# Kernel tuning notes

Measured on AMD Instinct MI355X. Metric: run time of the kernel, lower is better.

## Reference

```python
import jax, jax.numpy as jnp
import numpy as np

# config matching init_kwargs
B, LQ, LKV = 2, 1024, 1024
H, DQK, DV = 8, 64, 64
DQ = DK = DVIN = DOUT = 512
SPAN, STRIDE = 128, 1


def setup_inputs() -> dict:
    key = jax.random.key(0)
    ks = jax.random.split(key, 7)
    q = jax.random.normal(ks[0], (B, LQ, DQ), jnp.float32)
    k = jax.random.normal(ks[1], (B, LKV, DK), jnp.float32)
    v = jax.random.normal(ks[2], (B, LKV, DVIN), jnp.float32)
    # nn.Linear(bias=False) weights, stored as [in, out] for x @ W
    Wq = jax.random.normal(ks[3], (DQ, H * DQK), jnp.float32) / np.sqrt(DQ).astype(np.float32)
    Wk = jax.random.normal(ks[4], (DK, H * DQK), jnp.float32) / np.sqrt(DK).astype(np.float32)
    Wv = jax.random.normal(ks[5], (DVIN, H * DV), jnp.float32) / np.sqrt(DVIN).astype(np.float32)
    Wo = jax.random.normal(ks[6], (H * DV, DOUT), jnp.float32) / np.sqrt(H * DV).astype(np.float32)
    return dict(q=q, k=k, v=v, Wq=Wq, Wk=Wk, Wv=Wv, Wo=Wo)


def reference(q, k, v, Wq, Wk, Wv, Wo):
    b = q.shape[0]
    Q = (q @ Wq).reshape(b, LQ, H, DQK).transpose(0, 2, 1, 3)    # [b,H,LQ,DQK]
    K = (k @ Wk).reshape(b, LKV, H, DQK).transpose(0, 2, 1, 3)   # [b,H,LKV,DQK]
    V = (v @ Wv).reshape(b, LKV, H, DV).transpose(0, 2, 1, 3)    # [b,H,LKV,DV]

    # banded window indices: kvi[i, j] = i - (span-1) + stride*j
    row = jnp.arange(SPAN)[:, None]
    col = jnp.arange(LQ)[None, :]
    kvi = row - (SPAN - 1) + STRIDE * col                         # [SPAN, LQ]
    valid = (kvi >= 0) & (kvi < LKV)
    kvi_c = jnp.clip(kvi, 0, LKV - 1)

    Kw = K[:, :, kvi_c, :]                                        # [b,H,SPAN,LQ,DQK]
    scores = jnp.einsum('bhjd,bhsjd->bhsj', Q, Kw) / np.float32(np.sqrt(DQK))
    scores = jnp.where(valid[None, None], scores, -jnp.inf)
    w = jax.nn.softmax(scores, axis=2)                            # softmax over span (dim=2)

    Vw = V[:, :, kvi_c, :]                                        # [b,H,SPAN,LQ,DV]
    out_h = jnp.einsum('bhsj,bhsjd->bhjd', w, Vw)                 # [b,H,LQ,DV]
    out = out_h.transpose(0, 2, 1, 3).reshape(b, LQ, H * DV)
    return out @ Wo
```

## Files before the change

kernel.cpp:

```cpp
#include <hip/hip_runtime.h>
#include <hip/hip_bf16.h>

#define LQ 1024
#define NH 8
#define DHEAD 64
#define DMODEL 512
#define SPAN 128
#define MROWS 2048

typedef __attribute__((ext_vector_type(8))) short   bf16x8;
typedef __attribute__((ext_vector_type(4))) float   f32x4;
typedef __attribute__((ext_vector_type(8))) unsigned short us8;

static __device__ __forceinline__ unsigned short f2bf(float f) {
    union { __hip_bfloat16 h; unsigned short u; } cv;
    cv.h = __float2bfloat16(f);
    return cv.u;
}

static __device__ __forceinline__ void gload_lds16(const void* g, void* l) {
    __builtin_amdgcn_global_load_lds((const __attribute__((address_space(1))) void*)g,
                                     (__attribute__((address_space(3))) void*)l, 16, 0, 0);
}

__global__ __launch_bounds__(256) void transposeW(
    const float* __restrict__ W0, const float* __restrict__ W1,
    const float* __restrict__ W2, const float* __restrict__ W3,
    unsigned short* __restrict__ T0, unsigned short* __restrict__ T1,
    unsigned short* __restrict__ T2, unsigned short* __restrict__ T3)
{
    const float* W = blockIdx.z == 0 ? W0 : blockIdx.z == 1 ? W1 : blockIdx.z == 2 ? W2 : W3;
    unsigned short* T = blockIdx.z == 0 ? T0 : blockIdx.z == 1 ? T1 : blockIdx.z == 2 ? T2 : T3;
    __shared__ unsigned short sT[64][72];
    int c = threadIdx.x & 63;
    int r0 = (threadIdx.x >> 6) * 16;
    int n0 = blockIdx.x * 64, k0 = blockIdx.y * 64;
    #pragma unroll
    for (int i = 0; i < 16; ++i) {
        int r = r0 + i;
        sT[c][r] = f2bf(W[(size_t)(k0 + r) * DMODEL + n0 + c]);
    }
    __syncthreads();
    #pragma unroll
    for (int i = 0; i < 16; ++i) {
        int r = r0 + i;
        T[(size_t)(n0 + r) * DMODEL + k0 + c] = sT[r][c];
    }
}

__global__ __launch_bounds__(512, 4) void gemm_qkv(
    const float* __restrict__ q, const float* __restrict__ k, const float* __restrict__ v,
    const unsigned short* __restrict__ WtQ, const unsigned short* __restrict__ WtK,
    const unsigned short* __restrict__ WtV,
    unsigned short* __restrict__ Qp, unsigned short* __restrict__ Kp,
    unsigned short* __restrict__ Vt)
{
    __shared__ __align__(16) unsigned short As[2][2][4096];
    __shared__ __align__(16) unsigned short Bs[2][2][4096];

    const int z = blockIdx.z;
    const float* A = z == 0 ? q : (z == 1 ? k : v);
    const unsigned short* Bt = z == 0 ? WtQ : (z == 1 ? WtK : WtV);
    unsigned short* C = z == 0 ? Qp : (z == 1 ? Kp : Vt);
    const bool mode2 = (z == 2);

    const int tid = threadIdx.x;
    const int lane = tid & 63;
    const int w = tid >> 6;
    const int wg = w & 3;
    const int half = w >> 2;
    const int tidh = tid & 255;
    const int wm = wg >> 1, wn = wg & 1;
    const int m0 = blockIdx.y * 64;
    const int n0 = blockIdx.x * 64;

    const int srow = lane >> 3;
    const int sgrp = (lane & 7) ^ srow;

    f32x4 acc[2][2];
    #pragma unroll
    for (int i = 0; i < 2; ++i)
        #pragma unroll
        for (int j = 0; j < 2; ++j)
            acc[i][j] = f32x4{0.f, 0.f, 0.f, 0.f};

    auto stageB = [&](int buf, int ktg) {
        const int k0 = ktg * 64;
        #pragma unroll
        for (int cc = 0; cc < 2; ++cc) {
            int call = wg * 2 + cc;
            int row = call * 8 + srow;
            gload_lds16(Bt + (size_t)(n0 + row) * DMODEL + k0 + (sgrp << 3),
                        &Bs[half][buf][call * 512]);
        }
    };

    float4 areg[2][2];
    auto loadA = [&](int ktg) {
        const int k0 = ktg * 64;
        #pragma unroll
        for (int i = 0; i < 2; ++i) {
            int c = i * 256 + tidh;
            int row = c >> 3, g = c & 7;
            const float* p = A + (size_t)(m0 + row) * DMODEL + k0 + g * 8;
            areg[i][0] = *(const float4*)p;
            areg[i][1] = *(const float4*)(p + 4);
        }
    };
    auto writeA = [&](int buf) {
        #pragma unroll
        for (int i = 0; i < 2; ++i) {
            int c = i * 256 + tidh;
            int row = c >> 3, g = c & 7;
            us8 t;
            t[0] = f2bf(areg[i][0].x); t[1] = f2bf(areg[i][0].y);
            t[2] = f2bf(areg[i][0].z); t[3] = f2bf(areg[i][0].w);
            t[4] = f2bf(areg[i][1].x); t[5] = f2bf(areg[i][1].y);
            t[6] = f2bf(areg[i][1].z); t[7] = f2bf(areg[i][1].w);
            *(us8*)&As[half][buf][row * 64 + ((g ^ (row & 7)) << 3)] = t;
        }
    };

    const int frow = lane & 15;
    const int fkg  = lane >> 4;

    auto ldfrag = [&](const unsigned short* base, int rb, int ks) -> bf16x8 {
        int row = rb * 16 + frow;
        int kg = ks * 4 + fkg;
        int off = row * 64 + ((kg ^ (row & 7)) << 3);
        return *(const bf16x8*)&base[off];
    };

    const unsigned short* aB[2] = { mode2 ? Bs[half][0] : As[half][0],
                                    mode2 ? Bs[half][1] : As[half][1] };
    const unsigned short* bB[2] = { mode2 ? As[half][0] : Bs[half][0],
                                    mode2 ? As[half][1] : Bs[half][1] };
    const int ra = mode2 ? wn : wm;
    const int rb_ = mode2 ? wm : wn;

    const int ktbase = half * 4;
    loadA(ktbase);
    stageB(0, ktbase);
    writeA(0);
    __syncthreads();

    for (int t = 0; t < 4; ++t) {
        int buf = t & 1;
        if (t < 3) { loadA(ktbase + t + 1); stageB(buf ^ 1, ktbase + t + 1); }
        #pragma unroll
        for (int ks = 0; ks < 2; ++ks) {
            bf16x8 a0 = ldfrag(aB[buf], ra * 2 + 0, ks);
            bf16x8 a1 = ldfrag(aB[buf], ra * 2 + 1, ks);
            bf16x8 b0 = ldfrag(bB[buf], rb_ * 2 + 0, ks);
            bf16x8 b1 = ldfrag(bB[buf], rb_ * 2 + 1, ks);
            acc[0][0] = __builtin_amdgcn_mfma_f32_16x16x32_bf16(a0, b0, acc[0][0], 0, 0, 0);
            acc[0][1] = __builtin_amdgcn_mfma_f32_16x16x32_bf16(a0, b1, acc[0][1], 0, 0, 0);
            acc[1][0] = __builtin_amdgcn_mfma_f32_16x16x32_bf16(a1, b0, acc[1][0], 0, 0, 0);
            acc[1][1] = __builtin_amdgcn_mfma_f32_16x16x32_bf16(a1, b1, acc[1][1], 0, 0, 0);
        }
        if (t < 3) writeA(buf ^ 1);
        __syncthreads();
    }

    float* red = (float*)&As[0][0][0];
    if (half == 1) {
        int base = (wg * 64 + lane) * 17;
        #pragma unroll
        for (int i = 0; i < 2; ++i)
            #pragma unroll
            for (int j = 0; j < 2; ++j)
                #pragma unroll
                for (int r = 0; r < 4; ++r)
                    red[base + (i * 2 + j) * 4 + r] = acc[i][j][r];
    }
    __syncthreads();
    if (half == 0) {
        int base = (wg * 64 + lane) * 17;
        #pragma unroll
        for (int i = 0; i < 2; ++i)
            #pragma unroll
            for (int j = 0; j < 2; ++j)
                #pragma unroll
                for (int r = 0; r < 4; ++r)
                    acc[i][j][r] += red[base + (i * 2 + j) * 4 + r];

        #pragma unroll
        for (int i = 0; i < 2; ++i) {
            #pragma unroll
            for (int j = 0; j < 2; ++j) {
                #pragma unroll
                for (int r = 0; r < 4; ++r) {
                    if (mode2) {
                        int n = n0 + wn * 32 + i * 16 + (lane >> 4) * 4 + r;
                        int m = m0 + wm * 32 + j * 16 + (lane & 15);
                        int b = m >> 10, jq = m & 1023, h = n >> 6, d = n & 63;
                        C[(((size_t)(b * NH + h) * DHEAD) + d) * LQ + jq] = f2bf(acc[i][j][r]);
                    } else {
                        int m = m0 + wm * 32 + i * 16 + (lane >> 4) * 4 + r;
                        int n = n0 + wn * 32 + j * 16 + (lane & 15);
                        int b = m >> 10, jq = m & 1023, h = n >> 6, d = n & 63;
                        C[(((size_t)(b * NH + h) * LQ) + jq) * DHEAD + d] = f2bf(acc[i][j][r]);
                    }
                }
            }
        }
    }
}

__global__ __launch_bounds__(512, 4) void gemm_out(
    const unsigned short* __restrict__ A, const unsigned short* __restrict__ Bt,
    float* __restrict__ C)
{
    __shared__ __align__(16) unsigned short As[2][2][2048];
    __shared__ __align__(16) unsigned short Bs[2][2][4096];

    const int tid = threadIdx.x;
    const int lane = tid & 63;
    const int w = tid >> 6;
    const int wg = w & 3;
    const int half = w >> 2;
    const int m0 = blockIdx.y * 32;
    const int n0 = blockIdx.x * 64;

    const int srow = lane >> 3;
    const int sgrp = (lane & 7) ^ srow;

    f32x4 acc[2];
    acc[0] = f32x4{0.f, 0.f, 0.f, 0.f};
    acc[1] = f32x4{0.f, 0.f, 0.f, 0.f};

    auto stage = [&](int buf, int ktg) {
        const int k0 = ktg * 64;
        gload_lds16(A + (size_t)(m0 + wg * 8 + srow) * DMODEL + k0 + (sgrp << 3),
                    &As[half][buf][wg * 512]);
        #pragma unroll
        for (int cc = 0; cc < 2; ++cc) {
            int call = wg * 2 + cc;
            int row = call * 8 + srow;
            gload_lds16(Bt + (size_t)(n0 + row) * DMODEL + k0 + (sgrp << 3),
                        &Bs[half][buf][call * 512]);
        }
    };

    const int frow = lane & 15;
    const int fkg  = lane >> 4;

    auto ldfrag = [&](const unsigned short* base, int rb, int ks) -> bf16x8 {
        int row = rb * 16 + frow;
        int kg = ks * 4 + fkg;
        int off = row * 64 + ((kg ^ (row & 7)) << 3);
        return *(const bf16x8*)&base[off];
    };

    const int ktbase = half * 4;
    stage(0, ktbase);
    __syncthreads();

    for (int t = 0; t < 4; ++t) {
        int buf = t & 1;
        if (t < 3) stage(buf ^ 1, ktbase + t + 1);
        #pragma unroll
        for (int ks = 0; ks < 2; ++ks) {
            bf16x8 a0 = ldfrag(As[half][buf], 0, ks);
            bf16x8 a1 = ldfrag(As[half][buf], 1, ks);
            bf16x8 b0 = ldfrag(Bs[half][buf], wg, ks);
            acc[0] = __builtin_amdgcn_mfma_f32_16x16x32_bf16(a0, b0, acc[0], 0, 0, 0);
            acc[1] = __builtin_amdgcn_mfma_f32_16x16x32_bf16(a1, b0, acc[1], 0, 0, 0);
        }
        __syncthreads();
    }

    float* red = (float*)&As[0][0][0];
    if (half == 1) {
        int base = (wg * 64 + lane) * 9;
        #pragma unroll
        for (int i = 0; i < 2; ++i)
            #pragma unroll
            for (int r = 0; r < 4; ++r)
                red[base + i * 4 + r] = acc[i][r];
    }
    __syncthreads();
    if (half == 0) {
        int base = (wg * 64 + lane) * 9;
        #pragma unroll
        for (int i = 0; i < 2; ++i) {
            #pragma unroll
            for (int r = 0; r < 4; ++r) {
                float vsum = acc[i][r] + red[base + i * 4 + r];
                int m = m0 + i * 16 + (lane >> 4) * 4 + r;
                int n = n0 + wg * 16 + (lane & 15);
                C[(size_t)m * DMODEL + n] = vsum;
            }
        }
    }
}

__global__ __launch_bounds__(256) void attn_mfma(
    const unsigned short* __restrict__ Qp, const unsigned short* __restrict__ Kp,
    const unsigned short* __restrict__ Vt, unsigned short* __restrict__ O)
{
    __shared__ __align__(16) unsigned short Ks[192 * 64];
    __shared__ __align__(16) unsigned short Vs[64 * 192];
    __shared__ __align__(16) unsigned short Ps[64 * 200];

    const int tid = threadIdx.x;
    const int lane = tid & 63;
    const int w = tid >> 6;
    const int bh = blockIdx.y;
    const int j0 = blockIdx.x * 64;
    const int kv0 = j0 - 128;

    const unsigned short* Kg = Kp + (size_t)bh * LQ * DHEAD;
    const unsigned short* Vg = Vt + (size_t)bh * DHEAD * LQ;

    const us8 zz = {0, 0, 0, 0, 0, 0, 0, 0};

    us8 kreg[6];
    #pragma unroll
    for (int i = 0; i < 6; ++i) {
        int c = i * 256 + tid;
        int row = c >> 3, g = c & 7;
        int grow = kv0 + row;
        us8 t = zz;
        if (grow >= 0) t = *(const us8*)&Kg[(size_t)grow * DHEAD + g * 8];
        kreg[i] = t;
    }
    us8 vreg[6];
    #pragma unroll
    for (int i = 0; i < 6; ++i) {
        int c = i * 256 + tid;
        int d = c / 24, g = c - d * 24;
        int col = kv0 + g * 8;
        us8 t = zz;
        if (col >= 0) t = *(const us8*)&Vg[(size_t)d * LQ + col];
        vreg[i] = t;
    }
    #pragma unroll
    for (int i = 0; i < 6; ++i) {
        int c = i * 256 + tid;
        int row = c >> 3, g = c & 7;
        *(us8*)&Ks[row * 64 + ((g ^ (row & 7)) << 3)] = kreg[i];
    }
    #pragma unroll
    for (int i = 0; i < 6; ++i) {
        int c = i * 256 + tid;
        int d = c / 24, g = c - d * 24;
        int sg = (g & ~7) | ((g & 7) ^ (d & 7));
        *(us8*)&Vs[d * 192 + sg * 8] = vreg[i];
    }

    const int frow = lane & 15, fkg = lane >> 4;

    bf16x8 qa[2];
    {
        const unsigned short* Qrow = Qp + ((size_t)bh * LQ + j0 + w * 16 + frow) * DHEAD;
        qa[0] = *(const bf16x8*)&Qrow[fkg * 8];
        qa[1] = *(const bf16x8*)&Qrow[32 + fkg * 8];
    }

    __syncthreads();

    f32x4 sacc[12];
    #pragma unroll
    for (int b = 0; b < 12; ++b) sacc[b] = f32x4{0.f, 0.f, 0.f, 0.f};
    #pragma unroll
    for (int b = 0; b < 12; ++b) {
        #pragma unroll
        for (int ks = 0; ks < 2; ++ks) {
            int row = b * 16 + frow;
            int kg = ks * 4 + fkg;
            bf16x8 kb = *(const bf16x8*)&Ks[row * 64 + ((kg ^ (row & 7)) << 3)];
            sacc[b] = __builtin_amdgcn_mfma_f32_16x16x32_bf16(qa[ks], kb, sacc[b], 0, 0, 0);
        }
    }

    #pragma unroll
    for (int r = 0; r < 4; ++r) {
        int q = w * 16 + fkg * 4 + r;
        float sv[12];
        float mx = -1e30f;
        #pragma unroll
        for (int b = 0; b < 12; ++b) {
            int rel = b * 16 + frow - 128 - q;
            int kvabs = kv0 + b * 16 + frow;
            bool valid = (rel <= 0) & (rel >= -(SPAN - 1)) & (kvabs >= 0);
            float s = valid ? sacc[b][r] * 0.125f : -1e30f;
            sv[b] = s;
            mx = fmaxf(mx, s);
        }
        #pragma unroll
        for (int off = 1; off < 16; off <<= 1) mx = fmaxf(mx, __shfl_xor(mx, off));
        float sum = 0.f;
        #pragma unroll
        for (int b = 0; b < 12; ++b) { float p = __expf(sv[b] - mx); sv[b] = p; sum += p; }
        #pragma unroll
        for (int off = 1; off < 16; off <<= 1) sum += __shfl_xor(sum, off);
        float inv = 1.0f / sum;
        #pragma unroll
        for (int b = 0; b < 12; ++b) sacc[b][r] = sv[b] * inv;
    }

    #pragma unroll
    for (int b = 0; b < 12; ++b) {
        #pragma unroll
        for (int r = 0; r < 4; ++r) {
            int q = w * 16 + fkg * 4 + r;
            Ps[q * 200 + b * 16 + frow] = f2bf(sacc[b][r]);
        }
    }

    f32x4 oacc[4];
    #pragma unroll
    for (int nb = 0; nb < 4; ++nb) oacc[nb] = f32x4{0.f, 0.f, 0.f, 0.f};
    #pragma unroll
    for (int kb = 0; kb < 6; ++kb) {
        int q = w * 16 + frow;
        bf16x8 pa = *(const bf16x8*)&Ps[q * 200 + (kb * 4 + fkg) * 8];
        #pragma unroll
        for (int nb = 0; nb < 4; ++nb) {
            int d = nb * 16 + frow;
            int g = kb * 4 + fkg;
            int sg = (g & ~7) | ((g & 7) ^ (d & 7));
            bf16x8 vb = *(const bf16x8*)&Vs[d * 192 + sg * 8];
            oacc[nb] = __builtin_amdgcn_mfma_f32_16x16x32_bf16(pa, vb, oacc[nb], 0, 0, 0);
        }
    }

    int b = bh >> 3, h = bh & 7;
    #pragma unroll
    for (int nb = 0; nb < 4; ++nb) {
        #pragma unroll
        for (int r = 0; r < 4; ++r) {
            int jq = j0 + w * 16 + fkg * 4 + r;
            int col = h * 64 + nb * 16 + frow;
            O[(size_t)(b * LQ + jq) * DMODEL + col] = f2bf(oacc[nb][r]);
        }
    }
}

extern "C" void kernel_launch(void* const* d_in, const int* in_sizes, int n_in,
                              void* d_out, int out_size, void* d_ws, size_t ws_size,
                              hipStream_t stream) {
    const float* q  = (const float*)d_in[0];
    const float* k  = (const float*)d_in[1];
    const float* v  = (const float*)d_in[2];
    const float* Wq = (const float*)d_in[3];
    const float* Wk = (const float*)d_in[4];
    const float* Wv = (const float*)d_in[5];
    const float* Wo = (const float*)d_in[6];

    const size_t MK = (size_t)MROWS * DMODEL;
    const size_t WK = (size_t)DMODEL * DMODEL;

    unsigned short* WtQ = (unsigned short*)d_ws;
    unsigned short* WtK = WtQ + WK;
    unsigned short* WtV = WtK + WK;
    unsigned short* WtO = WtV + WK;
    unsigned short* Qp  = WtO + WK;
    unsigned short* Kp  = Qp + MK;
    unsigned short* Vt  = Kp + MK;
    unsigned short* Ah  = Vt + MK;

    transposeW<<<dim3(8, 8, 4), 256, 0, stream>>>(Wq, Wk, Wv, Wo, WtQ, WtK, WtV, WtO);

    gemm_qkv<<<dim3(8, 32, 3), 512, 0, stream>>>(q, k, v, WtQ, WtK, WtV, Qp, Kp, Vt);

    attn_mfma<<<dim3(LQ / 64, 16), 256, 0, stream>>>(Qp, Kp, Vt, Ah);

    gemm_out<<<dim3(8, 64), 512, 0, stream>>>(Ah, WtO, (float*)d_out);
}
```

Baseline: 41.48 us.

## Fuse output projection into attention kernel via per-head atomic accumulation

Removes the separate output-projection GEMM. Each attention block now multiplies its per-head 64x64 output tile by the matching 64-row slice of Wo, reading the weights straight from global memory, and atomically adds the partial result into the fp32 output. The output buffer is zeroed with a memset beforehand. This drops one kernel launch and the bf16 round trip of the attention output. In exchange it adds 8-way atomic contention per output element, uncached global weight loads, a memset, and a large live accumulator array that raises register pressure.

New measurement: 71.82 us. 73.2% more time.

```diff
diff --git a/kernel.cpp b/kernel.cpp
--- a/kernel.cpp
+++ b/kernel.cpp
@@ -207,101 +207,15 @@
     }
 }
 
-__global__ __launch_bounds__(512, 4) void gemm_out(
-    const unsigned short* __restrict__ A, const unsigned short* __restrict__ Bt,
-    float* __restrict__ C)
-{
-    __shared__ __align__(16) unsigned short As[2][2][2048];
-    __shared__ __align__(16) unsigned short Bs[2][2][4096];
-
-    const int tid = threadIdx.x;
-    const int lane = tid & 63;
-    const int w = tid >> 6;
-    const int wg = w & 3;
-    const int half = w >> 2;
-    const int m0 = blockIdx.y * 32;
-    const int n0 = blockIdx.x * 64;
-
-    const int srow = lane >> 3;
-    const int sgrp = (lane & 7) ^ srow;
-
-    f32x4 acc[2];
-    acc[0] = f32x4{0.f, 0.f, 0.f, 0.f};
-    acc[1] = f32x4{0.f, 0.f, 0.f, 0.f};
-
-    auto stage = [&](int buf, int ktg) {
-        const int k0 = ktg * 64;
-        gload_lds16(A + (size_t)(m0 + wg * 8 + srow) * DMODEL + k0 + (sgrp << 3),
-                    &As[half][buf][wg * 512]);
-        #pragma unroll
-        for (int cc = 0; cc < 2; ++cc) {
-            int call = wg * 2 + cc;
-            int row = call * 8 + srow;
-            gload_lds16(Bt + (size_t)(n0 + row) * DMODEL + k0 + (sgrp << 3),
-                        &Bs[half][buf][call * 512]);
-        }
-    };
-
-    const int frow = lane & 15;
-    const int fkg  = lane >> 4;
-
-    auto ldfrag = [&](const unsigned short* base, int rb, int ks) -> bf16x8 {
-        int row = rb * 16 + frow;
-        int kg = ks * 4 + fkg;
-        int off = row * 64 + ((kg ^ (row & 7)) << 3);
-        return *(const bf16x8*)&base[off];
-    };
-
-    const int ktbase = half * 4;
-    stage(0, ktbase);
-    __syncthreads();
-
-    for (int t = 0; t < 4; ++t) {
-        int buf = t & 1;
-        if (t < 3) stage(buf ^ 1, ktbase + t + 1);
-        #pragma unroll
-        for (int ks = 0; ks < 2; ++ks) {
-            bf16x8 a0 = ldfrag(As[half][buf], 0, ks);
-            bf16x8 a1 = ldfrag(As[half][buf], 1, ks);
-            bf16x8 b0 = ldfrag(Bs[half][buf], wg, ks);
-            acc[0] = __builtin_amdgcn_mfma_f32_16x16x32_bf16(a0, b0, acc[0], 0, 0, 0);
-            acc[1] = __builtin_amdgcn_mfma_f32_16x16x32_bf16(a1, b0, acc[1], 0, 0, 0);
-        }
-        __syncthreads();
-    }
-
-    float* red = (float*)&As[0][0][0];
-    if (half == 1) {
-        int base = (wg * 64 + lane) * 9;
-        #pragma unroll
-        for (int i = 0; i < 2; ++i)
-            #pragma unroll
-            for (int r = 0; r < 4; ++r)
-                red[base + i * 4 + r] = acc[i][r];
-    }
-    __syncthreads();
-    if (half == 0) {
-        int base = (wg * 64 + lane) * 9;
-        #pragma unroll
-        for (int i = 0; i < 2; ++i) {
-            #pragma unroll
-            for (int r = 0; r < 4; ++r) {
-                float vsum = acc[i][r] + red[base + i * 4 + r];
-                int m = m0 + i * 16 + (lane >> 4) * 4 + r;
-                int n = n0 + wg * 16 + (lane & 15);
-                C[(size_t)m * DMODEL + n] = vsum;
-            }
-        }
-    }
-}
-
-__global__ __launch_bounds__(256) void attn_mfma(
+__global__ __launch_bounds__(256) void attn_out(
     const unsigned short* __restrict__ Qp, const unsigned short* __restrict__ Kp,
-    const unsigned short* __restrict__ Vt, unsigned short* __restrict__ O)
+    const unsigned short* __restrict__ Vt, const unsigned short* __restrict__ WtO,
+    float* __restrict__ out)
 {
     __shared__ __align__(16) unsigned short Ks[192 * 64];
     __shared__ __align__(16) unsigned short Vs[64 * 192];
     __shared__ __align__(16) unsigned short Ps[64 * 200];
+    __shared__ __align__(16) unsigned short Os[64][72];
 
     const int tid = threadIdx.x;
     const int lane = tid & 63;
@@ -426,14 +340,39 @@
         }
     }
 
-    int b = bh >> 3, h = bh & 7;
+    const int b = bh >> 3, h = bh & 7;
     #pragma unroll
     for (int nb = 0; nb < 4; ++nb) {
         #pragma unroll
         for (int r = 0; r < 4; ++r) {
-            int jq = j0 + w * 16 + fkg * 4 + r;
-            int col = h * 64 + nb * 16 + frow;
-            O[(size_t)(b * LQ + jq) * DMODEL + col] = f2bf(oacc[nb][r]);
+            int q = w * 16 + fkg * 4 + r;
+            Os[q][nb * 16 + frow] = f2bf(oacc[nb][r]);
+        }
+    }
+
+    #pragma unroll
+    for (int p = 0; p < 2; ++p) {
+        f32x4 oc[16];
+        #pragma unroll
+        for (int t = 0; t < 16; ++t) oc[t] = f32x4{0.f, 0.f, 0.f, 0.f};
+        #pragma unroll
+        for (int ks = 0; ks < 2; ++ks) {
+            bf16x8 af = *(const bf16x8*)&Os[w * 16 + frow][(ks * 4 + fkg) * 8];
+            #pragma unroll
+            for (int t = 0; t < 16; ++t) {
+                int n = (p * 16 + t) * 16 + frow;
+                bf16x8 bw = *(const bf16x8*)&WtO[(size_t)n * DMODEL + h * 64 + (ks * 4 + fkg) * 8];
+                oc[t] = __builtin_amdgcn_mfma_f32_16x16x32_bf16(af, bw, oc[t], 0, 0, 0);
+            }
+        }
+        #pragma unroll
+        for (int t = 0; t < 16; ++t) {
+            #pragma unroll
+            for (int r = 0; r < 4; ++r) {
+                int m = b * LQ + j0 + w * 16 + fkg * 4 + r;
+                int n = (p * 16 + t) * 16 + frow;
+                atomicAdd(&out[(size_t)m * DMODEL + n], oc[t][r]);
+            }
         }
     }
 }
@@ -459,13 +398,12 @@
     unsigned short* Qp  = WtO + WK;
     unsigned short* Kp  = Qp + MK;
     unsigned short* Vt  = Kp + MK;
-    unsigned short* Ah  = Vt + MK;
+
+    hipMemsetAsync(d_out, 0, (size_t)MROWS * DMODEL * sizeof(float), stream);
 
     transposeW<<<dim3(8, 8, 4), 256, 0, stream>>>(Wq, Wk, Wv, Wo, WtQ, WtK, WtV, WtO);
 
     gemm_qkv<<<dim3(8, 32, 3), 512, 0, stream>>>(q, k, v, WtQ, WtK, WtV, Qp, Kp, Vt);
 
-    attn_mfma<<<dim3(LQ / 64, 16), 256, 0, stream>>>(Qp, Kp, Vt, Ah);
-
-    gemm_out<<<dim3(8, 64), 512, 0, stream>>>(Ah, WtO, (float*)d_out);
-}
+    attn_out<<<dim3(LQ / 64, 16), 256, 0, stream>>>(Qp, Kp, Vt, WtO, (float*)d_out);
+}
```
